# Optimization experiments

Hardware: AMD Instinct MI355X
Metric: run time of the kernel (lower is better)

Reference implementation:

```python
import jax, jax.numpy as jnp
import numpy as np

B, S, N = 16, 128, 64            # batch, sentence length, padded KB-word slots per sentence
E, DK, H, L = 128, 128, 128, 32  # char embed, kb embed, per-direction hidden (hidden_size=2H), labels
CHAR_NUM, KB_NUM = 8000, 200000


def setup_inputs():
    key = jax.random.key(0)
    ks = jax.random.split(key, 40)
    u = lambda k, sh: jax.random.uniform(k, sh, jnp.float32, -0.08, 0.08)
    inp = {
        "char_ids": jax.random.randint(ks[0], (B, S), 0, CHAR_NUM),
        "kb_word_ids": jax.random.randint(ks[1], (B, N), 0, KB_NUM),
        "word_begin": jax.random.randint(ks[2], (B, N), 0, S),
        "word_len": jax.random.randint(ks[3], (B, N), 0, 6),
        "label": jax.random.randint(ks[4], (B, S), 0, L),
        "sequence_length": jax.random.randint(ks[5], (B,), S // 2, S + 1),
        "char_emb": u(ks[6], (CHAR_NUM, E)),
        "kb_emb": u(ks[7], (KB_NUM, DK)),
        "dense_W": u(ks[8], (2 * H, L)),
        "dense_b": jnp.zeros((L,), jnp.float32),
        "crf_T": u(ks[9], (L, L)),
    }
    i = 10
    for p in ("f", "r"):
        inp[p + "_Wcx"] = u(ks[i], (E, 4 * H))
        inp[p + "_Wch"] = u(ks[i + 1], (H, 4 * H))
        inp[p + "_bc"] = jnp.zeros((4 * H,), jnp.float32)
        inp[p + "_Wwx"] = u(ks[i + 2], (DK, 3 * H))
        inp[p + "_Wwh"] = u(ks[i + 3], (H, 3 * H))
        inp[p + "_bw"] = jnp.zeros((3 * H,), jnp.float32)
        inp[p + "_Wlx"] = u(ks[i + 4], (E, H))
        inp[p + "_Wlc"] = u(ks[i + 5], (H, H))
        inp[p + "_bl"] = jnp.zeros((H,), jnp.float32)
        i += 6
    return inp


def _lattice_dir(X, Xw, begin, end, pos_valid, word_valid,
                 Wcx, Wch, bc, Wwx, Wwh, bw, Wlx, Wlc, bl):
    # X:[S,E] chars in scan order, Xw:[N,DK] KB words, begin/end:[N] span indices
    # in scan order (end inclusive), pos_valid:[S] bool, word_valid:[N] bool.
    Xg = X @ Wcx + bc    # [S,4H] hoisted char-gate input projection
    Xl = X @ Wlx + bl    # [S,H]  hoisted link-gate input projection
    Wg = Xw @ Wwx + bw   # [N,3H] hoisted word-gate input projection

    def step(carry, t):
        h_hist, c_hist = carry                 # [S+1,H]; slot k = state after step k-1
        h_prev, c_prev = h_hist[t], c_hist[t]
        gi, gf, go, gg = jnp.split(Xg[t] + h_prev @ Wch, 4)
        i = jax.nn.sigmoid(gi); f = jax.nn.sigmoid(gf)
        o = jax.nn.sigmoid(go); g = jnp.tanh(gg)
        # word cells: built from the state just before each word's begin position
        hb, cb = h_hist[begin], c_hist[begin]  # [N,H]
        wi, wf, wg = jnp.split(Wg + hb @ Wwh, 3, axis=1)
        cw = jax.nn.sigmoid(wf) * cb + jax.nn.sigmoid(wi) * jnp.tanh(wg)  # [N,H]
        lg = jax.nn.sigmoid(Xl[t] + cw @ Wlc)  # [N,H] link gates
        wmask = ((end == t) & word_valid).astype(X.dtype)[:, None]
        ew = jnp.exp(lg) * wmask
        ec = jnp.exp(i)
        c_lat = (ec * g + (ew * cw).sum(0)) / (ec + ew.sum(0))  # gate-normalized merge
        c_std = f * c_prev + i * g             # plain LSTM step when no word ends at t
        c_t = jnp.where(wmask.sum() > 0, c_lat, c_std)
        h_t = o * jnp.tanh(c_t)
        v = pos_valid[t]
        h_hist = h_hist.at[t + 1].set(jnp.where(v, h_t, h_prev))
        c_hist = c_hist.at[t + 1].set(jnp.where(v, c_t, c_prev))
        return (h_hist, c_hist), jnp.where(v, h_t, jnp.zeros_like(h_t))

    init = (jnp.zeros((S + 1, H), X.dtype), jnp.zeros((S + 1, H), X.dtype))
    _, hs = jax.lax.scan(step, init, jnp.arange(S))
    return hs  # [S,H]


def _forward(char_ids, kb_word_ids, word_begin, word_len, label, sequence_length,
             char_emb, kb_emb, dense_W, dense_b, crf_T, fparams, rparams):
    X = char_emb[char_ids]            # [B,S,E]
    Xw = kb_emb[kb_word_ids]          # [B,N,DK]
    end = jnp.minimum(word_begin + word_len, S - 1)   # inclusive span end
    word_valid = end < sequence_length[:, None]       # whole span inside sentence
    pos = jnp.arange(S)
    pv_f = pos[None, :] < sequence_length[:, None]
    fwd = jax.vmap(lambda x, xw, b, e, pv, wv:
                   _lattice_dir(x, xw, b, e, pv, wv, *fparams))(
        X, Xw, word_begin, end, pv_f, word_valid)
    # backward direction: flip time axis; span (b,e) maps to (S-1-e, S-1-b)
    pv_r = pos[None, :] >= (S - sequence_length)[:, None]
    bwd = jax.vmap(lambda x, xw, b, e, pv, wv:
                   _lattice_dir(x, xw, b, e, pv, wv, *rparams))(
        X[:, ::-1], Xw, S - 1 - end, S - 1 - word_begin, pv_r, word_valid)[:, ::-1]
    feats = jnp.concatenate([fwd, bwd], axis=-1)      # [B,S,2H]
    logits = feats @ dense_W + dense_b                # [B,S,L]
    # CRF negative log-likelihood
    mask = pv_f.astype(logits.dtype)                  # [B,S]
    emit = jnp.take_along_axis(logits, label[..., None], axis=2)[..., 0]
    trans = crf_T[label[:, :-1], label[:, 1:]]
    gold = (emit * mask).sum(1) + (trans * mask[:, 1:]).sum(1)

    def fstep(alpha, xs):
        logit_t, m_t = xs
        new = jax.scipy.special.logsumexp(alpha[:, :, None] + crf_T[None], axis=1) + logit_t
        return jnp.where(m_t[:, None] > 0, new, alpha), None

    alpha, _ = jax.lax.scan(fstep, logits[:, 0],
                            (logits[:, 1:].transpose(1, 0, 2), mask[:, 1:].T))
    logZ = jax.scipy.special.logsumexp(alpha, axis=1)
    return jnp.mean(logZ - gold)


def reference(char_ids, kb_word_ids, word_begin, word_len, label, sequence_length,
              char_emb, kb_emb, dense_W, dense_b, crf_T,
              f_Wcx, f_Wch, f_bc, f_Wwx, f_Wwh, f_bw, f_Wlx, f_Wlc, f_bl,
              r_Wcx, r_Wch, r_bc, r_Wwx, r_Wwh, r_bw, r_Wlx, r_Wlc, r_bl):
    fparams = (f_Wcx, f_Wch, f_bc, f_Wwx, f_Wwh, f_bw, f_Wlx, f_Wlc, f_bl)
    rparams = (r_Wcx, r_Wch, r_bc, r_Wwx, r_Wwh, r_bw, r_Wlx, r_Wlc, r_bl)
    return _forward(char_ids, kb_word_ids, word_begin, word_len, label, sequence_length,
                    char_emb, kb_emb, dense_W, dense_b, crf_T, fparams, rparams)
```

## Files before the change

kernel.cpp:

```cpp
#include <hip/hip_runtime.h>


typedef _Float16 f16x2 __attribute__((ext_vector_type(2)));

__device__ __forceinline__ float sigm(float x) { return 1.f / (1.f + __expf(-x)); }
__device__ __forceinline__ float tanh_fast(float x) {
    return 1.f - 2.f / (__expf(2.f * x) + 1.f);
}
__device__ __forceinline__ void bar_lgkm() {
    asm volatile("s_waitcnt lgkmcnt(0)\n\ts_barrier" ::: "memory");
}

#if defined(__has_builtin)
#if __has_builtin(__builtin_amdgcn_fdot2)
#define FDOT2(a, b, c) __builtin_amdgcn_fdot2((a), (b), (c), false)
#endif
#endif
#ifndef FDOT2
__device__ __forceinline__ float fdot2_sw(f16x2 a, f16x2 b, float c) {
    return fmaf((float)a.x, (float)b.x, fmaf((float)a.y, (float)b.y, c));
}
#define FDOT2(a, b, c) fdot2_sw((a), (b), (c))
#endif

#if defined(__has_builtin)
#if __has_builtin(__builtin_amdgcn_mov_dpp)
#define HAVE_DPP 1
#endif
#endif

__device__ __forceinline__ float quad_sum(float v) {
#ifdef HAVE_DPP
    v += __int_as_float(__builtin_amdgcn_mov_dpp(__float_as_int(v), 0xB1, 0xF, 0xF, true));
    v += __int_as_float(__builtin_amdgcn_mov_dpp(__float_as_int(v), 0x4E, 0xF, 0xF, true));
#else
    v += __shfl_xor(v, 1);
    v += __shfl_xor(v, 2);
#endif
    return v;
}

template <int K, int J, int RPB, int BLK>
__global__ __launch_bounds__(BLK)
void gemm_pair(const float* __restrict__ emb, const int* __restrict__ idx,
               const float* __restrict__ W0, const float* __restrict__ W1,
               const float* __restrict__ b0, const float* __restrict__ b1,
               float* __restrict__ out, int rowsTotal, int Sdim, int revmode)
{
    constexpr int NJ4 = J / 4;
    constexpr int RT  = BLK / NJ4;
    constexpr int RPT = RPB / RT;
    static_assert(BLK % NJ4 == 0 && RPB % RT == 0, "layout");
    const int y = blockIdx.y;
    const float* __restrict__ W    = y ? W1 : W0;
    const float* __restrict__ bias = y ? b1 : b0;
    float* __restrict__ outp = out + (size_t)y * rowsTotal * J;
    const int rev = (revmode && y) ? 1 : 0;

    __shared__ __align__(16) float xs[RPB * K];
    __shared__ const float* srcs[RPB];
    const int tid = threadIdx.x;
    const int r0 = blockIdx.x * RPB;
    if (tid < RPB) {
        const int row = r0 + tid;
        const float* s = nullptr;
        if (row < rowsTotal) {
            if (idx) {
                const int bb = row / Sdim, tt = row - bb * Sdim;
                const int ts = rev ? (Sdim - 1 - tt) : tt;
                s = emb + (size_t)idx[bb * Sdim + ts] * K;
            } else {
                s = emb + (size_t)row * K;
            }
        }
        srcs[tid] = s;
    }
    __syncthreads();
    constexpr int NQ = RPB * K / 4;
    for (int q = tid; q < NQ; q += BLK) {
        const int rr = q / (K / 4), qq = q - rr * (K / 4);
        const float4* s = (const float4*)srcs[rr];
        ((float4*)xs)[q] = s ? s[qq] : make_float4(0.f, 0.f, 0.f, 0.f);
    }
    __syncthreads();

    const int jq = tid % NJ4;
    const int rg = tid / NJ4;
    float4 acc[RPT];
#pragma unroll
    for (int r = 0; r < RPT; ++r) acc[r] = make_float4(0.f, 0.f, 0.f, 0.f);
    const float4* __restrict__ W4 = (const float4*)W;
#pragma unroll 4
    for (int k = 0; k < K; ++k) {
        const float4 wv = W4[(size_t)k * NJ4 + jq];
#pragma unroll
        for (int r = 0; r < RPT; ++r) {
            const float xv = xs[(rg * RPT + r) * K + k];
            acc[r].x = fmaf(xv, wv.x, acc[r].x);
            acc[r].y = fmaf(xv, wv.y, acc[r].y);
            acc[r].z = fmaf(xv, wv.z, acc[r].z);
            acc[r].w = fmaf(xv, wv.w, acc[r].w);
        }
    }
    const float4 bv = ((const float4*)bias)[jq];
#pragma unroll
    for (int r = 0; r < RPT; ++r) {
        const int row = r0 + rg * RPT + r;
        if (row < rowsTotal)
            ((float4*)outp)[(size_t)row * NJ4 + jq] =
                make_float4(acc[r].x + bv.x, acc[r].y + bv.y,
                            acc[r].z + bv.z, acc[r].w + bv.w);
    }
}

#define HH_BYTES (129 * 128 * 2)
#define CH_BYTES (129 * 128 * 4)
#define LAT_DYN_SMEM (HH_BYTES + CH_BYTES)

__global__ __launch_bounds__(512, 2)
void lattice_kernel(const float* __restrict__ Xg,
                    const float* __restrict__ Xl,
                    const float* __restrict__ Wgp,
                    const float* __restrict__ Wch_f, const float* __restrict__ Wch_r,
                    const float* __restrict__ Wwh_f, const float* __restrict__ Wwh_r,
                    const float* __restrict__ Wlc_f, const float* __restrict__ Wlc_r,
                    const int* __restrict__ word_begin, const int* __restrict__ word_len,
                    const int* __restrict__ seqlen,
                    float* __restrict__ feats)
{
    extern __shared__ __align__(16) char dyn_smem[];
    _Float16* hh = (_Float16*)dyn_smem;
    float*    ch = (float*)(dyn_smem + HH_BYTES);

    const int bdid = blockIdx.x;
    const int b = bdid >> 1, dir = bdid & 1;
    const int tid = threadIdx.x;
    const int kc  = tid & 3;
    const int jj  = tid >> 2;

    const float* Wch = dir ? Wch_r : Wch_f;
    const float* Wwh = dir ? Wwh_r : Wwh_f;
    const float* Wlc = dir ? Wlc_r : Wlc_f;

    f16x2 wch2[64];
    {
        const float* base = Wch + (size_t)(kc * 32) * 512 + jj;
#pragma unroll
        for (int g = 0; g < 4; ++g)
#pragma unroll
            for (int u2 = 0; u2 < 16; ++u2) {
                f16x2 v;
                v.x = (_Float16)base[(size_t)(2 * u2) * 512 + g * 128];
                v.y = (_Float16)base[(size_t)(2 * u2 + 1) * 512 + g * 128];
                wch2[g * 16 + u2] = v;
            }
    }
    f16x2 wwh2[48];
    {
        const float* base = Wwh + (size_t)(kc * 32) * 384 + jj;
#pragma unroll
        for (int g = 0; g < 3; ++g)
#pragma unroll
            for (int u2 = 0; u2 < 16; ++u2) {
                f16x2 v;
                v.x = (_Float16)base[(size_t)(2 * u2) * 384 + g * 128];
                v.y = (_Float16)base[(size_t)(2 * u2 + 1) * 384 + g * 128];
                wwh2[g * 16 + u2] = v;
            }
    }
    f16x2 wlc2[16];
    {
        const float* base = Wlc + (size_t)(kc * 32) * 128 + jj;
#pragma unroll
        for (int u2 = 0; u2 < 16; ++u2) {
            f16x2 v;
            v.x = (_Float16)base[(size_t)(2 * u2) * 128];
            v.y = (_Float16)base[(size_t)(2 * u2 + 1) * 128];
            wlc2[u2] = v;
        }
    }

    __shared__ _Float16 cw2s[2][2][128];
    __shared__ int ev_start[129];
    __shared__ int cnts[128];
    __shared__ int fills[128];
    __shared__ short ev_word[64];
    __shared__ short wbeg_s[64];

    const int sl = seqlen[b];

    if (tid < 128) { cnts[tid] = 0; fills[tid] = 0; }
    __syncthreads();
    int myvalid = 0, myed = 0;
    if (tid < 64) {
        const int bg = word_begin[b * 64 + tid];
        const int ln = word_len[b * 64 + tid];
        int ef = bg + ln; if (ef > 127) ef = 127;
        myvalid = (ef < sl);
        const int bd_ = dir ? (127 - ef) : bg;
        const int ed_ = dir ? (127 - bg) : ef;
        wbeg_s[tid] = (short)bd_;
        myed = ed_;
        if (myvalid) atomicAdd(&cnts[ed_], 1);
    }
    __syncthreads();
    if (tid == 0) {
        int run = 0; ev_start[0] = 0;
        for (int t = 0; t < 128; ++t) { run += cnts[t]; ev_start[t + 1] = run; }
    }
    __syncthreads();
    if (tid < 64 && myvalid) {
        const int pos = atomicAdd(&fills[myed], 1);
        ev_word[ev_start[myed] + pos] = (short)tid;
    }
    if (tid < 128) { hh[tid] = (_Float16)0.f; ch[tid] = 0.f; }
    __syncthreads();

    const float* Xg_b = Xg + ((size_t)dir * 2048 + (size_t)b * 128) * 512;
    const float* Xl_b = Xl + ((size_t)dir * 2048 + (size_t)b * 128) * 128;
    const float* Wg_b = Wgp + ((size_t)dir * 1024 + (size_t)b * 64) * 384;

    float h_reg = 0.f, c_reg = 0.f;
    const int xgoff = kc * 128 + jj;

    int   curE, cur_ec0;
    int   cur_bgs[2] = {0, 0};
    float cur_wgp[2][3] = {};
    float cur_xl = 0.f;
    float xg_cur;
    {
        const int e0 = ev_start[0];
        curE = ev_start[1] - e0;
        cur_ec0 = curE < 2 ? curE : 2;
#pragma unroll
        for (int s = 0; s < 2; ++s)
            if (s < cur_ec0) {
                const int w = ev_word[e0 + s];
                cur_bgs[s] = wbeg_s[w];
                const float* wgr = Wg_b + (size_t)w * 384;
                cur_wgp[s][0] = wgr[jj];
                cur_wgp[s][1] = wgr[128 + jj];
                cur_wgp[s][2] = wgr[256 + jj];
            }
        if (curE > 0) cur_xl = Xl_b[jj];
        xg_cur = Xg_b[xgoff];
    }

    for (int t = 0; t < 128; ++t) {
        int   nxtE = 0, nxt_ec0 = 0;
        int   nxt_bgs[2] = {0, 0};
        float nxt_wgp[2][3] = {};
        float nxt_xl = 0.f, xg_nxt = 0.f;
        if (t < 127) {
            const int e0n = ev_start[t + 1];
            nxtE = ev_start[t + 2] - e0n;
            nxt_ec0 = nxtE < 2 ? nxtE : 2;
#pragma unroll
            for (int s = 0; s < 2; ++s)
                if (s < nxt_ec0) {
                    const int w = ev_word[e0n + s];
                    nxt_bgs[s] = wbeg_s[w];
                    const float* wgr = Wg_b + (size_t)w * 384;
                    nxt_wgp[s][0] = wgr[jj];
                    nxt_wgp[s][1] = wgr[128 + jj];
                    nxt_wgp[s][2] = wgr[256 + jj];
                }
            if (nxtE > 0) nxt_xl = Xl_b[(size_t)(t + 1) * 128 + jj];
            xg_nxt = Xg_b[(size_t)(t + 1) * 512 + xgoff];
        }

        float p0 = 0.f, p1 = 0.f, p2 = 0.f, p3 = 0.f;
        {
            const f16x2* hrow = (const f16x2*)(hh + (size_t)t * 128) + kc * 16;
            f16x2 hv[16];
#pragma unroll
            for (int u2 = 0; u2 < 16; ++u2) hv[u2] = hrow[u2];
#pragma unroll
            for (int u2 = 0; u2 < 16; ++u2) {
                p0 = FDOT2(wch2[u2],      hv[u2], p0);
                p1 = FDOT2(wch2[16 + u2], hv[u2], p1);
                p2 = FDOT2(wch2[32 + u2], hv[u2], p2);
                p3 = FDOT2(wch2[48 + u2], hv[u2], p3);
            }
        }
        float q[2][3];
#pragma unroll
        for (int s = 0; s < 2; ++s) { q[s][0] = 0.f; q[s][1] = 0.f; q[s][2] = 0.f; }
#pragma unroll
        for (int s = 0; s < 2; ++s)
            if (s < cur_ec0) {
                const f16x2* hbrow = (const f16x2*)(hh + (size_t)cur_bgs[s] * 128) + kc * 16;
#pragma unroll
                for (int u2 = 0; u2 < 16; ++u2) {
                    const f16x2 hb = hbrow[u2];
                    q[s][0] = FDOT2(wwh2[u2],      hb, q[s][0]);
                    q[s][1] = FDOT2(wwh2[16 + u2], hb, q[s][1]);
                    q[s][2] = FDOT2(wwh2[32 + u2], hb, q[s][2]);
                }
            }

        if      (kc == 0) p0 += xg_cur;
        else if (kc == 1) p1 += xg_cur;
        else if (kc == 2) p2 += xg_cur;
        else              p3 += xg_cur;

        const float gi = sigm(quad_sum(p0));
        const float gf = sigm(quad_sum(p1));
        const float go = sigm(quad_sum(p2));
        const float gg = tanh_fast(quad_sum(p3));

        float accn = 0.f, accd = 0.f;
        if (curE > 0) {
            const int e0 = ev_start[t];
            float cwcur[2] = {0.f, 0.f};
#pragma unroll
            for (int s = 0; s < 2; ++s)
                if (s < cur_ec0) {
                    const float wi = cur_wgp[s][0] + quad_sum(q[s][0]);
                    const float wf = cur_wgp[s][1] + quad_sum(q[s][1]);
                    const float wv = cur_wgp[s][2] + quad_sum(q[s][2]);
                    const float cb = ch[(size_t)cur_bgs[s] * 128 + jj];
                    const float cwv = sigm(wf) * cb + sigm(wi) * tanh_fast(wv);
                    cwcur[s] = cwv;
                    if (kc == 0) cw2s[0][s][jj] = (_Float16)cwv;
                }
            bar_lgkm();
            const int nc = (curE + 1) >> 1;
            for (int c = 0; c < nc; ++c) {
                const int base2 = c * 2;
                const int en = (curE - base2) < 2 ? (curE - base2) : 2;
                float lgs[2] = {0.f, 0.f};
#pragma unroll
                for (int s = 0; s < 2; ++s)
                    if (s < en) {
                        const f16x2* cwrow = (const f16x2*)(&cw2s[c & 1][s][0]) + kc * 16;
                        float r = 0.f;
#pragma unroll
                        for (int u2 = 0; u2 < 16; ++u2) r = FDOT2(wlc2[u2], cwrow[u2], r);
                        lgs[s] = quad_sum(r);
                    }
                const int nb = base2 + 2;
                int nn = curE - nb; nn = nn < 0 ? 0 : (nn > 2 ? 2 : nn);
                float cwnxt[2] = {0.f, 0.f};
#pragma unroll
                for (int s = 0; s < 2; ++s)
                    if (s < nn) {
                        const int w = ev_word[e0 + nb + s];
                        const int bg2 = wbeg_s[w];
                        const float* wgr = Wg_b + (size_t)w * 384;
                        const float wg0 = wgr[jj], wg1 = wgr[128 + jj], wg2 = wgr[256 + jj];
                        const f16x2* hbrow = (const f16x2*)(hh + (size_t)bg2 * 128) + kc * 16;
                        float q0 = 0.f, q1 = 0.f, q2 = 0.f;
#pragma unroll
                        for (int u2 = 0; u2 < 16; ++u2) {
                            const f16x2 hb = hbrow[u2];
                            q0 = FDOT2(wwh2[u2],      hb, q0);
                            q1 = FDOT2(wwh2[16 + u2], hb, q1);
                            q2 = FDOT2(wwh2[32 + u2], hb, q2);
                        }
                        const float wi = wg0 + quad_sum(q0);
                        const float wf = wg1 + quad_sum(q1);
                        const float wv = wg2 + quad_sum(q2);
                        const float cb = ch[(size_t)bg2 * 128 + jj];
                        const float cwv = sigm(wf) * cb + sigm(wi) * tanh_fast(wv);
                        cwnxt[s] = cwv;
                        if (kc == 0) cw2s[(c + 1) & 1][s][jj] = (_Float16)cwv;
                    }
#pragma unroll
                for (int s = 0; s < 2; ++s)
                    if (s < en) {
                        const float lg = sigm(cur_xl + lgs[s]);
                        const float ew = __expf(lg);
                        accn = fmaf(ew, cwcur[s], accn);
                        accd += ew;
                    }
                if (c + 1 < nc) {
                    bar_lgkm();
                    cwcur[0] = cwnxt[0]; cwcur[1] = cwnxt[1];
                }
            }
        }

        float c_t;
        if (curE > 0) {
            const float ec = __expf(gi);
            c_t = (ec * gg + accn) / (ec + accd);
        } else {
            c_t = gf * c_reg + gi * gg;
        }
        const float h_t = go * tanh_fast(c_t);
        const bool v = dir ? (t >= 128 - sl) : (t < sl);
        const float hn = v ? h_t : h_reg;
        const float cn = v ? c_t : c_reg;
        h_reg = hn; c_reg = cn;
        if (kc == 0) {
            hh[(size_t)(t + 1) * 128 + jj] = (_Float16)hn;
            ch[(size_t)(t + 1) * 128 + jj] = cn;
        }

        curE = nxtE; cur_ec0 = nxt_ec0;
        cur_bgs[0] = nxt_bgs[0]; cur_bgs[1] = nxt_bgs[1];
#pragma unroll
        for (int s = 0; s < 2; ++s) {
            cur_wgp[s][0] = nxt_wgp[s][0];
            cur_wgp[s][1] = nxt_wgp[s][1];
            cur_wgp[s][2] = nxt_wgp[s][2];
        }
        cur_xl = nxt_xl;
        xg_cur = xg_nxt;
        bar_lgkm();
    }

    for (int i = tid; i < 128 * 128; i += 512) {
        const int t = i >> 7, j = i & 127;
        const bool v = dir ? (t >= 128 - sl) : (t < sl);
        const float hv = v ? (float)hh[(size_t)(t + 1) * 128 + j] : 0.f;
        const int s = dir ? (127 - t) : t;
        feats[((size_t)b * 128 + s) * 256 + dir * 128 + j] = hv;
    }
}

__global__ void crf_kernel(const float* __restrict__ logits,
                           const int* __restrict__ label,
                           const int* __restrict__ seqlen,
                           const float* __restrict__ T,
                           float* __restrict__ out_part)
{
    const int half = threadIdx.x >> 5;
    const int j    = threadIdx.x & 31;
    const int b    = blockIdx.x * 2 + half;

    float Tc[32];
#pragma unroll
    for (int i = 0; i < 32; ++i) Tc[i] = T[i * 32 + j];

    const float* lg = logits + (size_t)b * 128 * 32;
    const int* lab = label + b * 128;
    const int sl = seqlen[b];

    float g = 0.f;
#pragma unroll
    for (int r = 0; r < 4; ++r) {
        const int t = j + r * 32;
        if (t < sl) {
            g += lg[t * 32 + lab[t]];
            if (t >= 1) g += T[lab[t - 1] * 32 + lab[t]];
        }
    }
#pragma unroll
    for (int m = 16; m; m >>= 1) g += __shfl_xor(g, m, 32);

    __shared__ __align__(16) float alpha_s[2][32];
    float av = lg[j];
    alpha_s[half][j] = av;
    __syncthreads();
    for (int t = 1; t < 128; ++t) {
        float a[32];
        const float4* ap = (const float4*)alpha_s[half];
#pragma unroll
        for (int q = 0; q < 8; ++q) {
            const float4 v = ap[q];
            a[4 * q] = v.x; a[4 * q + 1] = v.y; a[4 * q + 2] = v.z; a[4 * q + 3] = v.w;
        }
        float m = -1e30f;
#pragma unroll
        for (int i = 0; i < 32; ++i) m = fmaxf(m, a[i] + Tc[i]);
        float s = 0.f;
#pragma unroll
        for (int i = 0; i < 32; ++i) s += __expf(a[i] + Tc[i] - m);
        float nv = m + __logf(s) + lg[t * 32 + j];
        if (t >= sl) nv = av;
        av = nv;
        __syncthreads();
        alpha_s[half][j] = av;
        __syncthreads();
    }
    float m2 = av;
#pragma unroll
    for (int m = 16; m; m >>= 1) m2 = fmaxf(m2, __shfl_xor(m2, m, 32));
    float s2 = __expf(av - m2);
#pragma unroll
    for (int m = 16; m; m >>= 1) s2 += __shfl_xor(s2, m, 32);
    if (j == 0) out_part[b] = (m2 + __logf(s2)) - g;
}

__global__ void finalize_kernel(const float* __restrict__ partb, float* __restrict__ out)
{
    if (threadIdx.x == 0 && blockIdx.x == 0) {
        float s = 0.f;
        for (int i = 0; i < 16; i++) s += partb[i];
        out[0] = s * (1.f / 16.f);
    }
}

extern "C" void kernel_launch(void* const* d_in, const int* in_sizes, int n_in,
                              void* d_out, int out_size, void* d_ws, size_t ws_size,
                              hipStream_t stream)
{
    (void)in_sizes; (void)n_in; (void)out_size; (void)ws_size;
    const int*   char_ids    = (const int*)d_in[0];
    const int*   kb_word_ids = (const int*)d_in[1];
    const int*   word_begin  = (const int*)d_in[2];
    const int*   word_len    = (const int*)d_in[3];
    const int*   label       = (const int*)d_in[4];
    const int*   seqlen      = (const int*)d_in[5];
    const float* char_emb    = (const float*)d_in[6];
    const float* kb_emb      = (const float*)d_in[7];
    const float* dense_W     = (const float*)d_in[8];
    const float* dense_b     = (const float*)d_in[9];
    const float* crf_T       = (const float*)d_in[10];
    const float* f_Wcx = (const float*)d_in[11];
    const float* f_Wch = (const float*)d_in[12];
    const float* f_bc  = (const float*)d_in[13];
    const float* f_Wwx = (const float*)d_in[14];
    const float* f_Wwh = (const float*)d_in[15];
    const float* f_bw  = (const float*)d_in[16];
    const float* f_Wlx = (const float*)d_in[17];
    const float* f_Wlc = (const float*)d_in[18];
    const float* f_bl  = (const float*)d_in[19];
    const float* r_Wcx = (const float*)d_in[20];
    const float* r_Wch = (const float*)d_in[21];
    const float* r_bc  = (const float*)d_in[22];
    const float* r_Wwx = (const float*)d_in[23];
    const float* r_Wwh = (const float*)d_in[24];
    const float* r_bw  = (const float*)d_in[25];
    const float* r_Wlx = (const float*)d_in[26];
    const float* r_Wlc = (const float*)d_in[27];
    const float* r_bl  = (const float*)d_in[28];

    float* ws = (float*)d_ws;
    size_t o = 0;
    float* Xg     = ws + o; o += (size_t)2 * 2048 * 512;
    float* Xl     = ws + o; o += (size_t)2 * 2048 * 128;
    float* Wg     = ws + o; o += (size_t)2 * 1024 * 384;
    float* feats  = ws + o; o += (size_t)2048 * 256;
    float* logits = ws + o; o += (size_t)2048 * 32;
    float* partb  = ws + o; o += 16;

    gemm_pair<128, 512, 8, 256><<<dim3(256, 2), 256, 0, stream>>>(
        char_emb, char_ids, f_Wcx, r_Wcx, f_bc, r_bc, Xg, 2048, 128, 1);
    gemm_pair<128, 128, 8, 256><<<dim3(256, 2), 256, 0, stream>>>(
        char_emb, char_ids, f_Wlx, r_Wlx, f_bl, r_bl, Xl, 2048, 128, 1);
    gemm_pair<128, 384, 8, 192><<<dim3(128, 2), 192, 0, stream>>>(
        kb_emb, kb_word_ids, f_Wwx, r_Wwx, f_bw, r_bw, Wg, 1024, 64, 0);

    lattice_kernel<<<32, 512, LAT_DYN_SMEM, stream>>>(
        Xg, Xl, Wg, f_Wch, r_Wch, f_Wwh, r_Wwh, f_Wlc, r_Wlc,
        word_begin, word_len, seqlen, feats);

    gemm_pair<256, 32, 16, 128><<<dim3(128, 1), 128, 0, stream>>>(
        feats, nullptr, dense_W, dense_W, dense_b, dense_b, logits, 2048, 128, 0);
    crf_kernel<<<8, 64, 0, stream>>>(logits, label, seqlen, crf_T, partb);
    finalize_kernel<<<1, 64, 0, stream>>>(partb, (float*)d_out);
}
```

Measured before the change: 523.2 us.

## Use MFMA 16x16x32 for lattice recurrent matvecs instead of fdot2 quads

Replaces the per-thread fdot2 matrix-vector products and quad reductions in the lattice LSTM recurrence with MFMA instructions. The hidden-state vector is broadcast as the A operand and the recurrent weights are held as register-resident B fragments. Each wave computes 16 output columns, and only row 0 of each MFMA result is used. This removes the DPP reductions and cuts instruction count per step. In exchange, most of the MFMA work is wasted because a single-row matvec is padded to 16 rows, and the latency of the dependent MFMA chains sits on the serial critical path.

```diff
diff --git a/kernel.cpp b/kernel.cpp
--- a/kernel.cpp
+++ b/kernel.cpp
@@ -1,7 +1,8 @@
 #include <hip/hip_runtime.h>
 
 
-typedef _Float16 f16x2 __attribute__((ext_vector_type(2)));
+typedef _Float16 f16x8 __attribute__((ext_vector_type(8)));
+typedef float    f32x4 __attribute__((ext_vector_type(4)));
 
 __device__ __forceinline__ float sigm(float x) { return 1.f / (1.f + __expf(-x)); }
 __device__ __forceinline__ float tanh_fast(float x) {
@@ -11,33 +12,8 @@
     asm volatile("s_waitcnt lgkmcnt(0)\n\ts_barrier" ::: "memory");
 }
 
-#if defined(__has_builtin)
-#if __has_builtin(__builtin_amdgcn_fdot2)
-#define FDOT2(a, b, c) __builtin_amdgcn_fdot2((a), (b), (c), false)
-#endif
-#endif
-#ifndef FDOT2
-__device__ __forceinline__ float fdot2_sw(f16x2 a, f16x2 b, float c) {
-    return fmaf((float)a.x, (float)b.x, fmaf((float)a.y, (float)b.y, c));
-}
-#define FDOT2(a, b, c) fdot2_sw((a), (b), (c))
-#endif
-
-#if defined(__has_builtin)
-#if __has_builtin(__builtin_amdgcn_mov_dpp)
-#define HAVE_DPP 1
-#endif
-#endif
-
-__device__ __forceinline__ float quad_sum(float v) {
-#ifdef HAVE_DPP
-    v += __int_as_float(__builtin_amdgcn_mov_dpp(__float_as_int(v), 0xB1, 0xF, 0xF, true));
-    v += __int_as_float(__builtin_amdgcn_mov_dpp(__float_as_int(v), 0x4E, 0xF, 0xF, true));
-#else
-    v += __shfl_xor(v, 1);
-    v += __shfl_xor(v, 2);
-#endif
-    return v;
+__device__ __forceinline__ f32x4 mfma16(f16x8 a, f16x8 b, f32x4 c) {
+    return __builtin_amdgcn_mfma_f32_16x16x32_f16(a, b, c, 0, 0, 0);
 }
 
 template <int K, int J, int RPB, int BLK>
@@ -135,52 +111,48 @@
     const int bdid = blockIdx.x;
     const int b = bdid >> 1, dir = bdid & 1;
     const int tid = threadIdx.x;
-    const int kc  = tid & 3;
-    const int jj  = tid >> 2;
+    const int wid = tid >> 6;
+    const int ln  = tid & 63;
+    const int lg  = ln >> 4;
+    const int jm  = wid * 16 + (ln & 15);
 
     const float* Wch = dir ? Wch_r : Wch_f;
     const float* Wwh = dir ? Wwh_r : Wwh_f;
     const float* Wlc = dir ? Wlc_r : Wlc_f;
 
-    f16x2 wch2[64];
-    {
-        const float* base = Wch + (size_t)(kc * 32) * 512 + jj;
-#pragma unroll
-        for (int g = 0; g < 4; ++g)
-#pragma unroll
-            for (int u2 = 0; u2 < 16; ++u2) {
-                f16x2 v;
-                v.x = (_Float16)base[(size_t)(2 * u2) * 512 + g * 128];
-                v.y = (_Float16)base[(size_t)(2 * u2 + 1) * 512 + g * 128];
-                wch2[g * 16 + u2] = v;
-            }
-    }
-    f16x2 wwh2[48];
-    {
-        const float* base = Wwh + (size_t)(kc * 32) * 384 + jj;
-#pragma unroll
-        for (int g = 0; g < 3; ++g)
-#pragma unroll
-            for (int u2 = 0; u2 < 16; ++u2) {
-                f16x2 v;
-                v.x = (_Float16)base[(size_t)(2 * u2) * 384 + g * 128];
-                v.y = (_Float16)base[(size_t)(2 * u2 + 1) * 384 + g * 128];
-                wwh2[g * 16 + u2] = v;
-            }
-    }
-    f16x2 wlc2[16];
-    {
-        const float* base = Wlc + (size_t)(kc * 32) * 128 + jj;
-#pragma unroll
-        for (int u2 = 0; u2 < 16; ++u2) {
-            f16x2 v;
-            v.x = (_Float16)base[(size_t)(2 * u2) * 128];
-            v.y = (_Float16)base[(size_t)(2 * u2 + 1) * 128];
-            wlc2[u2] = v;
-        }
-    }
-
-    __shared__ _Float16 cw2s[2][2][128];
+    f16x8 Bc[4][4];
+#pragma unroll
+    for (int g = 0; g < 4; ++g)
+#pragma unroll
+        for (int kt = 0; kt < 4; ++kt) {
+            f16x8 v;
+#pragma unroll
+            for (int i = 0; i < 8; ++i)
+                v[i] = (_Float16)Wch[(size_t)(kt * 32 + lg * 8 + i) * 512 + (g * 128 + jm)];
+            Bc[g][kt] = v;
+        }
+    f16x8 Bw[3][4];
+#pragma unroll
+    for (int p = 0; p < 3; ++p)
+#pragma unroll
+        for (int kt = 0; kt < 4; ++kt) {
+            f16x8 v;
+#pragma unroll
+            for (int i = 0; i < 8; ++i)
+                v[i] = (_Float16)Wwh[(size_t)(kt * 32 + lg * 8 + i) * 384 + (p * 128 + jm)];
+            Bw[p][kt] = v;
+        }
+    f16x8 Bl[4];
+#pragma unroll
+    for (int kt = 0; kt < 4; ++kt) {
+        f16x8 v;
+#pragma unroll
+        for (int i = 0; i < 8; ++i)
+            v[i] = (_Float16)Wlc[(size_t)(kt * 32 + lg * 8 + i) * 128 + jm];
+        Bl[kt] = v;
+    }
+
+    __shared__ __align__(16) _Float16 cw2s[2][2][128];
     __shared__ int ev_start[129];
     __shared__ int cnts[128];
     __shared__ int fills[128];
@@ -194,8 +166,8 @@
     int myvalid = 0, myed = 0;
     if (tid < 64) {
         const int bg = word_begin[b * 64 + tid];
-        const int ln = word_len[b * 64 + tid];
-        int ef = bg + ln; if (ef > 127) ef = 127;
+        const int lnw = word_len[b * 64 + tid];
+        int ef = bg + lnw; if (ef > 127) ef = 127;
         myvalid = (ef < sl);
         const int bd_ = dir ? (127 - ef) : bg;
         const int ed_ = dir ? (127 - bg) : ef;
@@ -221,36 +193,36 @@
     const float* Wg_b = Wgp + ((size_t)dir * 1024 + (size_t)b * 64) * 384;
 
     float h_reg = 0.f, c_reg = 0.f;
-    const int xgoff = kc * 128 + jj;
 
     int   curE, cur_ec0;
     int   cur_bgs[2] = {0, 0};
     float cur_wgp[2][3] = {};
     float cur_xl = 0.f;
-    float xg_cur;
+    float xg_cur[4];
     {
-        const int e0 = ev_start[0];
-        curE = ev_start[1] - e0;
+        curE = ev_start[1];
         cur_ec0 = curE < 2 ? curE : 2;
 #pragma unroll
         for (int s = 0; s < 2; ++s)
             if (s < cur_ec0) {
-                const int w = ev_word[e0 + s];
-                cur_bgs[s] = wbeg_s[w];
-                const float* wgr = Wg_b + (size_t)w * 384;
-                cur_wgp[s][0] = wgr[jj];
-                cur_wgp[s][1] = wgr[128 + jj];
-                cur_wgp[s][2] = wgr[256 + jj];
+                const int wd = ev_word[s];
+                cur_bgs[s] = wbeg_s[wd];
+                const float* wgr = Wg_b + (size_t)wd * 384;
+                cur_wgp[s][0] = wgr[jm];
+                cur_wgp[s][1] = wgr[128 + jm];
+                cur_wgp[s][2] = wgr[256 + jm];
             }
-        if (curE > 0) cur_xl = Xl_b[jj];
-        xg_cur = Xg_b[xgoff];
+        if (curE > 0) cur_xl = Xl_b[jm];
+#pragma unroll
+        for (int g = 0; g < 4; ++g) xg_cur[g] = Xg_b[g * 128 + jm];
     }
 
     for (int t = 0; t < 128; ++t) {
         int   nxtE = 0, nxt_ec0 = 0;
         int   nxt_bgs[2] = {0, 0};
         float nxt_wgp[2][3] = {};
-        float nxt_xl = 0.f, xg_nxt = 0.f;
+        float nxt_xl = 0.f;
+        float xg_nxt[4] = {0.f, 0.f, 0.f, 0.f};
         if (t < 127) {
             const int e0n = ev_start[t + 1];
             nxtE = ev_start[t + 2] - e0n;
@@ -258,71 +230,63 @@
 #pragma unroll
             for (int s = 0; s < 2; ++s)
                 if (s < nxt_ec0) {
-                    const int w = ev_word[e0n + s];
-                    nxt_bgs[s] = wbeg_s[w];
-                    const float* wgr = Wg_b + (size_t)w * 384;
-                    nxt_wgp[s][0] = wgr[jj];
-                    nxt_wgp[s][1] = wgr[128 + jj];
-                    nxt_wgp[s][2] = wgr[256 + jj];
+                    const int wd = ev_word[e0n + s];
+                    nxt_bgs[s] = wbeg_s[wd];
+                    const float* wgr = Wg_b + (size_t)wd * 384;
+                    nxt_wgp[s][0] = wgr[jm];
+                    nxt_wgp[s][1] = wgr[128 + jm];
+                    nxt_wgp[s][2] = wgr[256 + jm];
                 }
-            if (nxtE > 0) nxt_xl = Xl_b[(size_t)(t + 1) * 128 + jj];
-            xg_nxt = Xg_b[(size_t)(t + 1) * 512 + xgoff];
-        }
-
-        float p0 = 0.f, p1 = 0.f, p2 = 0.f, p3 = 0.f;
-        {
-            const f16x2* hrow = (const f16x2*)(hh + (size_t)t * 128) + kc * 16;
-            f16x2 hv[16];
-#pragma unroll
-            for (int u2 = 0; u2 < 16; ++u2) hv[u2] = hrow[u2];
-#pragma unroll
-            for (int u2 = 0; u2 < 16; ++u2) {
-                p0 = FDOT2(wch2[u2],      hv[u2], p0);
-                p1 = FDOT2(wch2[16 + u2], hv[u2], p1);
-                p2 = FDOT2(wch2[32 + u2], hv[u2], p2);
-                p3 = FDOT2(wch2[48 + u2], hv[u2], p3);
-            }
-        }
-        float q[2][3];
-#pragma unroll
-        for (int s = 0; s < 2; ++s) { q[s][0] = 0.f; q[s][1] = 0.f; q[s][2] = 0.f; }
-#pragma unroll
-        for (int s = 0; s < 2; ++s)
-            if (s < cur_ec0) {
-                const f16x2* hbrow = (const f16x2*)(hh + (size_t)cur_bgs[s] * 128) + kc * 16;
-#pragma unroll
-                for (int u2 = 0; u2 < 16; ++u2) {
-                    const f16x2 hb = hbrow[u2];
-                    q[s][0] = FDOT2(wwh2[u2],      hb, q[s][0]);
-                    q[s][1] = FDOT2(wwh2[16 + u2], hb, q[s][1]);
-                    q[s][2] = FDOT2(wwh2[32 + u2], hb, q[s][2]);
-                }
-            }
-
-        if      (kc == 0) p0 += xg_cur;
-        else if (kc == 1) p1 += xg_cur;
-        else if (kc == 2) p2 += xg_cur;
-        else              p3 += xg_cur;
-
-        const float gi = sigm(quad_sum(p0));
-        const float gf = sigm(quad_sum(p1));
-        const float go = sigm(quad_sum(p2));
-        const float gg = tanh_fast(quad_sum(p3));
+            if (nxtE > 0) nxt_xl = Xl_b[(size_t)(t + 1) * 128 + jm];
+#pragma unroll
+            for (int g = 0; g < 4; ++g)
+                xg_nxt[g] = Xg_b[(size_t)(t + 1) * 512 + g * 128 + jm];
+        }
+
+        f16x8 A[4];
+#pragma unroll
+        for (int kt = 0; kt < 4; ++kt)
+            A[kt] = ((const f16x8*)hh)[t * 16 + kt * 4 + lg];
+        f32x4 d[4];
+#pragma unroll
+        for (int g = 0; g < 4; ++g) d[g] = (f32x4){0.f, 0.f, 0.f, 0.f};
+#pragma unroll
+        for (int kt = 0; kt < 4; ++kt)
+#pragma unroll
+            for (int g = 0; g < 4; ++g)
+                d[g] = mfma16(A[kt], Bc[g][kt], d[g]);
+
+        const float gi = sigm(d[0][0] + xg_cur[0]);
+        const float gf = sigm(d[1][0] + xg_cur[1]);
+        const float go = sigm(d[2][0] + xg_cur[2]);
+        const float gg = tanh_fast(d[3][0] + xg_cur[3]);
 
         float accn = 0.f, accd = 0.f;
         if (curE > 0) {
             const int e0 = ev_start[t];
-            float cwcur[2] = {0.f, 0.f};
+            float cwreg[2] = {0.f, 0.f};
 #pragma unroll
             for (int s = 0; s < 2; ++s)
                 if (s < cur_ec0) {
-                    const float wi = cur_wgp[s][0] + quad_sum(q[s][0]);
-                    const float wf = cur_wgp[s][1] + quad_sum(q[s][1]);
-                    const float wv = cur_wgp[s][2] + quad_sum(q[s][2]);
-                    const float cb = ch[(size_t)cur_bgs[s] * 128 + jj];
+                    f16x8 Ab[4];
+#pragma unroll
+                    for (int kt = 0; kt < 4; ++kt)
+                        Ab[kt] = ((const f16x8*)hh)[cur_bgs[s] * 16 + kt * 4 + lg];
+                    f32x4 ep[3];
+#pragma unroll
+                    for (int p = 0; p < 3; ++p) ep[p] = (f32x4){0.f, 0.f, 0.f, 0.f};
+#pragma unroll
+                    for (int kt = 0; kt < 4; ++kt)
+#pragma unroll
+                        for (int p = 0; p < 3; ++p)
+                            ep[p] = mfma16(Ab[kt], Bw[p][kt], ep[p]);
+                    const float wi = cur_wgp[s][0] + ep[0][0];
+                    const float wf = cur_wgp[s][1] + ep[1][0];
+                    const float wv = cur_wgp[s][2] + ep[2][0];
+                    const float cb = ch[(size_t)cur_bgs[s] * 128 + jm];
                     const float cwv = sigm(wf) * cb + sigm(wi) * tanh_fast(wv);
-                    cwcur[s] = cwv;
-                    if (kc == 0) cw2s[0][s][jj] = (_Float16)cwv;
+                    cwreg[s] = cwv;
+                    if (ln < 16) cw2s[0][s][jm] = (_Float16)cwv;
                 }
             bar_lgkm();
             const int nc = (curE + 1) >> 1;
@@ -333,50 +297,57 @@
 #pragma unroll
                 for (int s = 0; s < 2; ++s)
                     if (s < en) {
-                        const f16x2* cwrow = (const f16x2*)(&cw2s[c & 1][s][0]) + kc * 16;
-                        float r = 0.f;
-#pragma unroll
-                        for (int u2 = 0; u2 < 16; ++u2) r = FDOT2(wlc2[u2], cwrow[u2], r);
-                        lgs[s] = quad_sum(r);
+                        f16x8 Ac[4];
+#pragma unroll
+                        for (int kt = 0; kt < 4; ++kt)
+                            Ac[kt] = ((const f16x8*)(&cw2s[c & 1][s][0]))[kt * 4 + lg];
+                        f32x4 r = (f32x4){0.f, 0.f, 0.f, 0.f};
+#pragma unroll
+                        for (int kt = 0; kt < 4; ++kt)
+                            r = mfma16(Ac[kt], Bl[kt], r);
+                        lgs[s] = r[0];
                     }
                 const int nb = base2 + 2;
                 int nn = curE - nb; nn = nn < 0 ? 0 : (nn > 2 ? 2 : nn);
-                float cwnxt[2] = {0.f, 0.f};
+                float cwn[2] = {0.f, 0.f};
 #pragma unroll
                 for (int s = 0; s < 2; ++s)
                     if (s < nn) {
-                        const int w = ev_word[e0 + nb + s];
-                        const int bg2 = wbeg_s[w];
-                        const float* wgr = Wg_b + (size_t)w * 384;
-                        const float wg0 = wgr[jj], wg1 = wgr[128 + jj], wg2 = wgr[256 + jj];
-                        const f16x2* hbrow = (const f16x2*)(hh + (size_t)bg2 * 128) + kc * 16;
-                        float q0 = 0.f, q1 = 0.f, q2 = 0.f;
-#pragma unroll
-                        for (int u2 = 0; u2 < 16; ++u2) {
-                            const f16x2 hb = hbrow[u2];
-                            q0 = FDOT2(wwh2[u2],      hb, q0);
-                            q1 = FDOT2(wwh2[16 + u2], hb, q1);
-                            q2 = FDOT2(wwh2[32 + u2], hb, q2);
-                        }
-                        const float wi = wg0 + quad_sum(q0);
-                        const float wf = wg1 + quad_sum(q1);
-                        const float wv = wg2 + quad_sum(q2);
-                        const float cb = ch[(size_t)bg2 * 128 + jj];
+                        const int wd = ev_word[e0 + nb + s];
+                        const int bg2 = wbeg_s[wd];
+                        const float* wgr = Wg_b + (size_t)wd * 384;
+                        const float wg0 = wgr[jm], wg1 = wgr[128 + jm], wg2 = wgr[256 + jm];
+                        f16x8 Ab[4];
+#pragma unroll
+                        for (int kt = 0; kt < 4; ++kt)
+                            Ab[kt] = ((const f16x8*)hh)[bg2 * 16 + kt * 4 + lg];
+                        f32x4 ep[3];
+#pragma unroll
+                        for (int p = 0; p < 3; ++p) ep[p] = (f32x4){0.f, 0.f, 0.f, 0.f};
+#pragma unroll
+                        for (int kt = 0; kt < 4; ++kt)
+#pragma unroll
+                            for (int p = 0; p < 3; ++p)
+                                ep[p] = mfma16(Ab[kt], Bw[p][kt], ep[p]);
+                        const float wi = wg0 + ep[0][0];
+                        const float wf = wg1 + ep[1][0];
+                        const float wv = wg2 + ep[2][0];
+                        const float cb = ch[(size_t)bg2 * 128 + jm];
                         const float cwv = sigm(wf) * cb + sigm(wi) * tanh_fast(wv);
-                        cwnxt[s] = cwv;
-                        if (kc == 0) cw2s[(c + 1) & 1][s][jj] = (_Float16)cwv;
+                        cwn[s] = cwv;
+                        if (ln < 16) cw2s[(c + 1) & 1][s][jm] = (_Float16)cwv;
                     }
 #pragma unroll
                 for (int s = 0; s < 2; ++s)
                     if (s < en) {
-                        const float lg = sigm(cur_xl + lgs[s]);
-                        const float ew = __expf(lg);
-                        accn = fmaf(ew, cwcur[s], accn);
+                        const float lgv = sigm(cur_xl + lgs[s]);
+                        const float ew = __expf(lgv);
+                        accn = fmaf(ew, cwreg[s], accn);
                         accd += ew;
                     }
                 if (c + 1 < nc) {
                     bar_lgkm();
-                    cwcur[0] = cwnxt[0]; cwcur[1] = cwnxt[1];
+                    cwreg[0] = cwn[0]; cwreg[1] = cwn[1];
                 }
             }
         }
@@ -393,9 +364,9 @@
         const float hn = v ? h_t : h_reg;
         const float cn = v ? c_t : c_reg;
         h_reg = hn; c_reg = cn;
-        if (kc == 0) {
-            hh[(size_t)(t + 1) * 128 + jj] = (_Float16)hn;
-            ch[(size_t)(t + 1) * 128 + jj] = cn;
+        if (ln < 16) {
+            hh[(size_t)(t + 1) * 128 + jm] = (_Float16)hn;
+            ch[(size_t)(t + 1) * 128 + jm] = cn;
         }
 
         curE = nxtE; cur_ec0 = nxt_ec0;
@@ -407,7 +378,8 @@
             cur_wgp[s][2] = nxt_wgp[s][2];
         }
         cur_xl = nxt_xl;
-        xg_cur = xg_nxt;
+#pragma unroll
+        for (int g = 0; g < 4; ++g) xg_cur[g] = xg_nxt[g];
         bar_lgkm();
     }
 
```

Result: no change. 518.6 us (-0.9%).
